# Kernel tuning notes

Measured on AMD Instinct MI355X. Metric: run time of the kernel, lower is better.

## Reference

```python
import jax, jax.numpy as jnp
import numpy as np

B, T, D, H, OUT = 1024, 2048, 5, 64, 128


def _lstm_layer(x, Wih, Whh, bih, bhh):
    """PyTorch-convention LSTM layer. x: [B,T,Din]; gate order i,f,g,o."""
    b, t = x.shape[0], x.shape[1]
    h = Whh.shape[1]
    # Precompute input projections for all timesteps (the only big GEMM).
    xp = jnp.einsum('btd,gd->btg', x, Wih) + bih + bhh        # [B,T,4H]
    xp = jnp.swapaxes(xp, 0, 1)                               # [T,B,4H]

    def step(carry, xt):
        hprev, cprev = carry
        gates = xt + hprev @ Whh.T                            # [B,4H]
        i, f, g, o = jnp.split(gates, 4, axis=-1)
        i = jax.nn.sigmoid(i)
        f = jax.nn.sigmoid(f)
        g = jnp.tanh(g)
        o = jax.nn.sigmoid(o)
        c = f * cprev + i * g
        hnew = o * jnp.tanh(c)
        return (hnew, c), hnew

    h0 = jnp.zeros((b, h), x.dtype)
    (hT, cT), hs = jax.lax.scan(step, (h0, h0), xp)
    return jnp.swapaxes(hs, 0, 1), hT                         # [B,T,H], [B,H]


def setup_inputs() -> dict:
    key = jax.random.key(0)
    ks = jax.random.split(key, 11)
    s = 1.0 / np.sqrt(H)  # PyTorch LSTM init range

    def u(k, shape):
        return jax.random.uniform(k, shape, jnp.float32, -s, s)

    return {
        'x': jax.random.normal(ks[0], (B, T, D), jnp.float32),
        'W_ih0': u(ks[1], (4 * H, D)),
        'W_hh0': u(ks[2], (4 * H, H)),
        'b_ih0': u(ks[3], (4 * H,)),
        'b_hh0': u(ks[4], (4 * H,)),
        'W_ih1': u(ks[5], (4 * H, H)),
        'W_hh1': u(ks[6], (4 * H, H)),
        'b_ih1': u(ks[7], (4 * H,)),
        'b_hh1': u(ks[8], (4 * H,)),
        'W_fc': u(ks[9], (OUT, H)),
        'b_fc': u(ks[10], (OUT,)),
    }


def reference(x, W_ih0, W_hh0, b_ih0, b_hh0, W_ih1, W_hh1, b_ih1, b_hh1, W_fc, b_fc):
    # Layer 1 over raw 5-dim signal; inter-layer dropout is inactive at inference.
    y1, _ = _lstm_layer(x, W_ih0, W_hh0, b_ih0, b_hh0)
    # Layer 2; only its final hidden state hn[-1] is used downstream.
    _, h2 = _lstm_layer(y1, W_ih1, W_hh1, b_ih1, b_hh1)
    return jax.nn.relu(h2 @ W_fc.T + b_fc)                    # [B,128]
```

## Files before the change

kernel.cpp:

```cpp
#include <hip/hip_runtime.h>
#include <math.h>

#define BATCH 1024
#define TSEQ  2048
#define DIN   5
#define H     64
#define BT    4
#define SSTR  144
#define NOUT  128

typedef _Float16 f16x8 __attribute__((ext_vector_type(8)));
typedef float    f32x4 __attribute__((ext_vector_type(4)));

#if __has_builtin(__builtin_amdgcn_rcpf)
__device__ __forceinline__ float rcp_fast(float x) { return __builtin_amdgcn_rcpf(x); }
#else
__device__ __forceinline__ float rcp_fast(float x) { return 1.0f / x; }
#endif

#define LOG2E 1.44269504088896f

__device__ __forceinline__ float sigm2(float s) {
    return rcp_fast(1.0f + __builtin_amdgcn_exp2f(-s));
}
__device__ __forceinline__ float tanh2(float s) {
    return fmaf(-2.0f, rcp_fast(__builtin_amdgcn_exp2f(s) + 1.0f), 1.0f);
}

__global__ __launch_bounds__(512)
void lstm_mfma(const float* __restrict__ x,
               const float* __restrict__ Wih0, const float* __restrict__ Whh0,
               const float* __restrict__ bih0, const float* __restrict__ bhh0,
               const float* __restrict__ Wih1, const float* __restrict__ Whh1,
               const float* __restrict__ bih1, const float* __restrict__ bhh1,
               const float* __restrict__ Wfc,  const float* __restrict__ bfc,
               float* __restrict__ out)
{
    __shared__ alignas(16) _Float16 S[2][BT * SSTR];
    __shared__ alignas(16) float    h2f[BT][H];

    const int tid  = threadIdx.x;
    const int w    = tid >> 6;
    const int lane = tid & 63;
    const int col  = lane & 15;
    const int q    = lane >> 4;
    const int ww   = w & 3;
    const int lay  = w >> 2;
    const int hu   = 16 * ww + col;
    const int b0   = blockIdx.x * BT;

    for (int j = tid; j < 2 * BT * SSTR; j += 512)
        ((_Float16*)S)[j] = (_Float16)0.0f;

    const float sgl[4] = {LOG2E, LOG2E, 2.0f * LOG2E, LOG2E};

    f16x8 Bf[4][4];
    f32x4 bC[4];
    #pragma unroll
    for (int g = 0; g < 4; ++g) {
        const int   row = g * 64 + hu;
        const float sg  = sgl[g];
        const float* Wa = lay ? (Wih1 + row * H) : (Whh0 + row * H);
        f16x8 f0, f1, f2, f3;
        #pragma unroll
        for (int j = 0; j < 8; ++j) {
            f0[j] = (_Float16)(Wa[q * 8 + j] * sg);
            f1[j] = (_Float16)(Wa[32 + q * 8 + j] * sg);
        }
        if (lay) {
            const float* Wb = Whh1 + row * H;
            #pragma unroll
            for (int j = 0; j < 8; ++j) {
                f2[j] = (_Float16)(Wb[q * 8 + j] * sg);
                f3[j] = (_Float16)(Wb[32 + q * 8 + j] * sg);
            }
        } else {
            #pragma unroll
            for (int j = 0; j < 8; ++j) {
                const int kk = q * 8 + j;
                f2[j] = (_Float16)(kk < DIN ? Wih0[row * DIN + kk] * sg : 0.0f);
                f3[j] = (_Float16)0.0f;
            }
        }
        Bf[g][0] = f0; Bf[g][1] = f1; Bf[g][2] = f2; Bf[g][3] = f3;
        const float bb = (lay ? (bih1[row] + bhh1[row])
                              : (bih0[row] + bhh0[row])) * sg;
        bC[g] = f32x4{bb, bb, bb, bb};
    }

    const float* xp = x + (size_t)(b0 + (col >> 2)) * TSEQ * DIN;
    f16x8 ax = {(_Float16)0.0f, (_Float16)0.0f, (_Float16)0.0f, (_Float16)0.0f,
                (_Float16)0.0f, (_Float16)0.0f, (_Float16)0.0f, (_Float16)0.0f};
    f32x4 dx[4];
    if (lay == 0) {
        if (q == 0) {
            ax[0] = (_Float16)xp[0]; ax[1] = (_Float16)xp[1];
            ax[2] = (_Float16)xp[2]; ax[3] = (_Float16)xp[3];
            ax[4] = (_Float16)xp[4];
        }
        #pragma unroll
        for (int g = 0; g < 4; ++g)
            dx[g] = __builtin_amdgcn_mfma_f32_16x16x32_f16(ax, Bf[g][2], bC[g], 0, 0, 0);
        xp += DIN;
    }

    const int ab  = (col >> 2) * SSTR + q * 8;
    const int wb1 = q * SSTR + hu;
    const int wb2 = q * SSTR + 64 + hu;
    float cst = 0.0f, h2fin = 0.0f;

    __syncthreads();

    #pragma unroll 1
    for (int i = 0; i <= TSEQ; ++i) {
        const _Float16* rb = S[(i + 1) & 1];
        _Float16*       wbuf = S[i & 1];

        if (lay == 0) {
            const bool xld = (q == 0) && (i + 1 < TSEQ);
            float x0, x1, x2, x3, x4;
            if (xld) { x0 = xp[0]; x1 = xp[1]; x2 = xp[2]; x3 = xp[3]; x4 = xp[4]; }

            f16x8 a0 = *(const f16x8*)&rb[ab];
            f16x8 a1 = *(const f16x8*)&rb[ab + 32];
            f32x4 d[4];
            #pragma unroll
            for (int g = 0; g < 4; ++g) {
                d[g] = __builtin_amdgcn_mfma_f32_16x16x32_f16(a0, Bf[g][0], dx[g], 0, 0, 0);
                d[g] = __builtin_amdgcn_mfma_f32_16x16x32_f16(a1, Bf[g][1], d[g], 0, 0, 0);
            }
            if (i < TSEQ) {
                float iv = sigm2(d[0][0]);
                float fv = sigm2(d[1][0]);
                float gv = tanh2(d[2][0]);
                float ov = sigm2(d[3][0]);
                cst = fmaf(fv, cst, iv * gv);
                wbuf[wb1] = (_Float16)(ov * tanh2(2.0f * LOG2E * cst));
            }
            if (xld) {
                ax[0] = (_Float16)x0; ax[1] = (_Float16)x1;
                ax[2] = (_Float16)x2; ax[3] = (_Float16)x3;
                ax[4] = (_Float16)x4;
            }
            #pragma unroll
            for (int g = 0; g < 4; ++g)
                dx[g] = __builtin_amdgcn_mfma_f32_16x16x32_f16(ax, Bf[g][2], bC[g], 0, 0, 0);
            xp += DIN;
        } else {
            f16x8 ay0 = *(const f16x8*)&rb[ab];
            f16x8 ay1 = *(const f16x8*)&rb[ab + 32];
            f16x8 ah0 = *(const f16x8*)&rb[ab + 64];
            f16x8 ah1 = *(const f16x8*)&rb[ab + 96];
            f32x4 d[4];
            #pragma unroll
            for (int g = 0; g < 4; ++g) {
                d[g] = __builtin_amdgcn_mfma_f32_16x16x32_f16(ay0, Bf[g][0], bC[g], 0, 0, 0);
                d[g] = __builtin_amdgcn_mfma_f32_16x16x32_f16(ay1, Bf[g][1], d[g], 0, 0, 0);
                d[g] = __builtin_amdgcn_mfma_f32_16x16x32_f16(ah0, Bf[g][2], d[g], 0, 0, 0);
                d[g] = __builtin_amdgcn_mfma_f32_16x16x32_f16(ah1, Bf[g][3], d[g], 0, 0, 0);
            }
            if (i > 0) {
                float iv = sigm2(d[0][0]);
                float fv = sigm2(d[1][0]);
                float gv = tanh2(d[2][0]);
                float ov = sigm2(d[3][0]);
                cst = fmaf(fv, cst, iv * gv);
                h2fin = ov * tanh2(2.0f * LOG2E * cst);
                wbuf[wb2] = (_Float16)h2fin;
            }
        }
        __syncthreads();
    }

    if (lay) h2f[q][hu] = h2fin;
    __syncthreads();
    {
        const int e = tid >> 7;
        const int o = tid & (NOUT - 1);
        const float4* wr = (const float4*)(Wfc + o * H);
        const float*  hv = h2f[e];
        float s0 = 0.f, s1 = 0.f, s2 = 0.f, s3 = 0.f;
        #pragma unroll
        for (int k = 0; k < H / 4; ++k) {
            float4 wv = wr[k];
            s0 = fmaf(wv.x, hv[4 * k + 0], s0);
            s1 = fmaf(wv.y, hv[4 * k + 1], s1);
            s2 = fmaf(wv.z, hv[4 * k + 2], s2);
            s3 = fmaf(wv.w, hv[4 * k + 3], s3);
        }
        float acc = bfc[o] + (s0 + s1) + (s2 + s3);
        out[(size_t)(b0 + e) * NOUT + o] = fmaxf(acc, 0.0f);
    }
}

extern "C" void kernel_launch(void* const* d_in, const int* in_sizes, int n_in,
                              void* d_out, int out_size, void* d_ws, size_t ws_size,
                              hipStream_t stream) {
    const float* x    = (const float*)d_in[0];
    const float* Wih0 = (const float*)d_in[1];
    const float* Whh0 = (const float*)d_in[2];
    const float* bih0 = (const float*)d_in[3];
    const float* bhh0 = (const float*)d_in[4];
    const float* Wih1 = (const float*)d_in[5];
    const float* Whh1 = (const float*)d_in[6];
    const float* bih1 = (const float*)d_in[7];
    const float* bhh1 = (const float*)d_in[8];
    const float* Wfc  = (const float*)d_in[9];
    const float* bfc  = (const float*)d_in[10];
    float* out = (float*)d_out;

    lstm_mfma<<<dim3(BATCH / BT), dim3(512), 0, stream>>>(
        x, Wih0, Whh0, bih0, bhh0, Wih1, Whh1, bih1, bhh1, Wfc, bfc, out);
}
```

Before: 979.1 us.

## Merge both LSTM layers into each wave, halving block size to 256 threads

Instead of dedicating four waves to layer 1 and four to layer 2, each of four waves now computes both layers' gates for its hidden units in the same wavefront-pipelined step. Each wave holds all weight fragments in registers and issues the layer-1, layer-2 input and layer-2 recurrent MFMAs as independent chains, and the x loads are reorganized. This halves the waves per block, aiming to cut barrier cost and let the MFMA chains overlap within a wave. In exchange it raises register pressure and per-wave serial work, and the launch bound of one block per SIMD may limit occupancy.

```diff
diff --git a/kernel.cpp b/kernel.cpp
--- a/kernel.cpp
+++ b/kernel.cpp
@@ -19,6 +19,7 @@
 #endif
 
 #define LOG2E 1.44269504088896f
+#define MFMA16(A, B, C) __builtin_amdgcn_mfma_f32_16x16x32_f16((A), (B), (C), 0, 0, 0)
 
 __device__ __forceinline__ float sigm2(float s) {
     return rcp_fast(1.0f + __builtin_amdgcn_exp2f(-s));
@@ -27,7 +28,7 @@
     return fmaf(-2.0f, rcp_fast(__builtin_amdgcn_exp2f(s) + 1.0f), 1.0f);
 }
 
-__global__ __launch_bounds__(512)
+__global__ __launch_bounds__(256, 1)
 void lstm_mfma(const float* __restrict__ x,
                const float* __restrict__ Wih0, const float* __restrict__ Whh0,
                const float* __restrict__ bih0, const float* __restrict__ bhh0,
@@ -40,156 +41,140 @@
     __shared__ alignas(16) float    h2f[BT][H];
 
     const int tid  = threadIdx.x;
-    const int w    = tid >> 6;
+    const int ww   = tid >> 6;
     const int lane = tid & 63;
     const int col  = lane & 15;
     const int q    = lane >> 4;
-    const int ww   = w & 3;
-    const int lay  = w >> 2;
     const int hu   = 16 * ww + col;
     const int b0   = blockIdx.x * BT;
 
-    for (int j = tid; j < 2 * BT * SSTR; j += 512)
+    for (int j = tid; j < 2 * BT * SSTR; j += 256)
         ((_Float16*)S)[j] = (_Float16)0.0f;
 
     const float sgl[4] = {LOG2E, LOG2E, 2.0f * LOG2E, LOG2E};
 
-    f16x8 Bf[4][4];
-    f32x4 bC[4];
+    f16x8 Bh[4][2];
+    f16x8 Bx[4];
+    f16x8 C2[4][4];
+    f32x4 bC1[4], bC2[4];
     #pragma unroll
     for (int g = 0; g < 4; ++g) {
         const int   row = g * 64 + hu;
         const float sg  = sgl[g];
-        const float* Wa = lay ? (Wih1 + row * H) : (Whh0 + row * H);
-        f16x8 f0, f1, f2, f3;
+        const float* wh0 = Whh0 + row * H;
+        const float* wi1 = Wih1 + row * H;
+        const float* wh1 = Whh1 + row * H;
         #pragma unroll
         for (int j = 0; j < 8; ++j) {
-            f0[j] = (_Float16)(Wa[q * 8 + j] * sg);
-            f1[j] = (_Float16)(Wa[32 + q * 8 + j] * sg);
+            const int k = q * 8 + j;
+            Bh[g][0][j] = (_Float16)(wh0[k]      * sg);
+            Bh[g][1][j] = (_Float16)(wh0[32 + k] * sg);
+            C2[g][0][j] = (_Float16)(wi1[k]      * sg);
+            C2[g][1][j] = (_Float16)(wi1[32 + k] * sg);
+            C2[g][2][j] = (_Float16)(wh1[k]      * sg);
+            C2[g][3][j] = (_Float16)(wh1[32 + k] * sg);
+            Bx[g][j]    = (_Float16)(k < DIN ? Wih0[row * DIN + k] * sg : 0.0f);
         }
-        if (lay) {
-            const float* Wb = Whh1 + row * H;
-            #pragma unroll
-            for (int j = 0; j < 8; ++j) {
-                f2[j] = (_Float16)(Wb[q * 8 + j] * sg);
-                f3[j] = (_Float16)(Wb[32 + q * 8 + j] * sg);
-            }
-        } else {
-            #pragma unroll
-            for (int j = 0; j < 8; ++j) {
-                const int kk = q * 8 + j;
-                f2[j] = (_Float16)(kk < DIN ? Wih0[row * DIN + kk] * sg : 0.0f);
-                f3[j] = (_Float16)0.0f;
-            }
-        }
-        Bf[g][0] = f0; Bf[g][1] = f1; Bf[g][2] = f2; Bf[g][3] = f3;
-        const float bb = (lay ? (bih1[row] + bhh1[row])
-                              : (bih0[row] + bhh0[row])) * sg;
-        bC[g] = f32x4{bb, bb, bb, bb};
+        const float b1 = (bih0[row] + bhh0[row]) * sg;
+        const float b2 = (bih1[row] + bhh1[row]) * sg;
+        bC1[g] = f32x4{b1, b1, b1, b1};
+        bC2[g] = f32x4{b2, b2, b2, b2};
     }
 
     const float* xp = x + (size_t)(b0 + (col >> 2)) * TSEQ * DIN;
+    float x0 = 0.f, x1 = 0.f, x2 = 0.f, x3 = 0.f, x4 = 0.f;
+    if (q == 0) { x0 = xp[0]; x1 = xp[1]; x2 = xp[2]; x3 = xp[3]; x4 = xp[4]; }
+    xp += DIN;
+
     f16x8 ax = {(_Float16)0.0f, (_Float16)0.0f, (_Float16)0.0f, (_Float16)0.0f,
                 (_Float16)0.0f, (_Float16)0.0f, (_Float16)0.0f, (_Float16)0.0f};
-    f32x4 dx[4];
-    if (lay == 0) {
-        if (q == 0) {
-            ax[0] = (_Float16)xp[0]; ax[1] = (_Float16)xp[1];
-            ax[2] = (_Float16)xp[2]; ax[3] = (_Float16)xp[3];
-            ax[4] = (_Float16)xp[4];
-        }
-        #pragma unroll
-        for (int g = 0; g < 4; ++g)
-            dx[g] = __builtin_amdgcn_mfma_f32_16x16x32_f16(ax, Bf[g][2], bC[g], 0, 0, 0);
-        xp += DIN;
-    }
 
     const int ab  = (col >> 2) * SSTR + q * 8;
     const int wb1 = q * SSTR + hu;
     const int wb2 = q * SSTR + 64 + hu;
-    float cst = 0.0f, h2fin = 0.0f;
+    float cst1 = 0.f, cst2 = 0.f, h2fin = 0.f;
 
     __syncthreads();
 
     #pragma unroll 1
     for (int i = 0; i <= TSEQ; ++i) {
-        const _Float16* rb = S[(i + 1) & 1];
+        const _Float16* rb   = S[(i + 1) & 1];
         _Float16*       wbuf = S[i & 1];
 
-        if (lay == 0) {
-            const bool xld = (q == 0) && (i + 1 < TSEQ);
-            float x0, x1, x2, x3, x4;
-            if (xld) { x0 = xp[0]; x1 = xp[1]; x2 = xp[2]; x3 = xp[3]; x4 = xp[4]; }
+        f16x8 a0  = *(const f16x8*)&rb[ab];
+        f16x8 a1  = *(const f16x8*)&rb[ab + 32];
+        f16x8 ah0 = *(const f16x8*)&rb[ab + 64];
+        f16x8 ah1 = *(const f16x8*)&rb[ab + 96];
 
-            f16x8 a0 = *(const f16x8*)&rb[ab];
-            f16x8 a1 = *(const f16x8*)&rb[ab + 32];
-            f32x4 d[4];
-            #pragma unroll
-            for (int g = 0; g < 4; ++g) {
-                d[g] = __builtin_amdgcn_mfma_f32_16x16x32_f16(a0, Bf[g][0], dx[g], 0, 0, 0);
-                d[g] = __builtin_amdgcn_mfma_f32_16x16x32_f16(a1, Bf[g][1], d[g], 0, 0, 0);
-            }
-            if (i < TSEQ) {
-                float iv = sigm2(d[0][0]);
-                float fv = sigm2(d[1][0]);
-                float gv = tanh2(d[2][0]);
-                float ov = sigm2(d[3][0]);
-                cst = fmaf(fv, cst, iv * gv);
-                wbuf[wb1] = (_Float16)(ov * tanh2(2.0f * LOG2E * cst));
-            }
-            if (xld) {
-                ax[0] = (_Float16)x0; ax[1] = (_Float16)x1;
-                ax[2] = (_Float16)x2; ax[3] = (_Float16)x3;
-                ax[4] = (_Float16)x4;
-            }
-            #pragma unroll
-            for (int g = 0; g < 4; ++g)
-                dx[g] = __builtin_amdgcn_mfma_f32_16x16x32_f16(ax, Bf[g][2], bC[g], 0, 0, 0);
-            xp += DIN;
-        } else {
-            f16x8 ay0 = *(const f16x8*)&rb[ab];
-            f16x8 ay1 = *(const f16x8*)&rb[ab + 32];
-            f16x8 ah0 = *(const f16x8*)&rb[ab + 64];
-            f16x8 ah1 = *(const f16x8*)&rb[ab + 96];
-            f32x4 d[4];
-            #pragma unroll
-            for (int g = 0; g < 4; ++g) {
-                d[g] = __builtin_amdgcn_mfma_f32_16x16x32_f16(ay0, Bf[g][0], bC[g], 0, 0, 0);
-                d[g] = __builtin_amdgcn_mfma_f32_16x16x32_f16(ay1, Bf[g][1], d[g], 0, 0, 0);
-                d[g] = __builtin_amdgcn_mfma_f32_16x16x32_f16(ah0, Bf[g][2], d[g], 0, 0, 0);
-                d[g] = __builtin_amdgcn_mfma_f32_16x16x32_f16(ah1, Bf[g][3], d[g], 0, 0, 0);
-            }
-            if (i > 0) {
-                float iv = sigm2(d[0][0]);
-                float fv = sigm2(d[1][0]);
-                float gv = tanh2(d[2][0]);
-                float ov = sigm2(d[3][0]);
-                cst = fmaf(fv, cst, iv * gv);
-                h2fin = ov * tanh2(2.0f * LOG2E * cst);
-                wbuf[wb2] = (_Float16)h2fin;
-            }
+        if (q == 0) {
+            ax[0] = (_Float16)x0; ax[1] = (_Float16)x1; ax[2] = (_Float16)x2;
+            ax[3] = (_Float16)x3; ax[4] = (_Float16)x4;
+        }
+        f32x4 dx[4];
+        #pragma unroll
+        for (int g = 0; g < 4; ++g)
+            dx[g] = MFMA16(ax, Bx[g], bC1[g]);
+
+        if (q == 0 && i + 1 < TSEQ) { x0 = xp[0]; x1 = xp[1]; x2 = xp[2]; x3 = xp[3]; x4 = xp[4]; }
+        xp += DIN;
+
+        f32x4 d[4], e2[4], f2[4];
+        const f32x4 z4 = {0.f, 0.f, 0.f, 0.f};
+        #pragma unroll
+        for (int g = 0; g < 4; ++g) {
+            d[g]  = MFMA16(a0,  Bh[g][0], dx[g]);
+            d[g]  = MFMA16(a1,  Bh[g][1], d[g]);
+            e2[g] = MFMA16(a0,  C2[g][0], bC2[g]);
+            e2[g] = MFMA16(a1,  C2[g][1], e2[g]);
+            f2[g] = MFMA16(ah0, C2[g][2], z4);
+            f2[g] = MFMA16(ah1, C2[g][3], f2[g]);
+        }
+
+        if (i < TSEQ) {
+            float iv = sigm2(d[0][0]);
+            float fv = sigm2(d[1][0]);
+            float gv = tanh2(d[2][0]);
+            float ov = sigm2(d[3][0]);
+            cst1 = fmaf(fv, cst1, iv * gv);
+            wbuf[wb1] = (_Float16)(ov * tanh2(2.0f * LOG2E * cst1));
+        }
+        if (i > 0) {
+            float p0 = e2[0][0] + f2[0][0];
+            float p1 = e2[1][0] + f2[1][0];
+            float p2 = e2[2][0] + f2[2][0];
+            float p3 = e2[3][0] + f2[3][0];
+            float iv = sigm2(p0);
+            float fv = sigm2(p1);
+            float gv = tanh2(p2);
+            float ov = sigm2(p3);
+            cst2 = fmaf(fv, cst2, iv * gv);
+            h2fin = ov * tanh2(2.0f * LOG2E * cst2);
+            wbuf[wb2] = (_Float16)h2fin;
         }
         __syncthreads();
     }
 
-    if (lay) h2f[q][hu] = h2fin;
+    h2f[q][hu] = h2fin;
     __syncthreads();
     {
-        const int e = tid >> 7;
-        const int o = tid & (NOUT - 1);
+        const int o  = tid & (NOUT - 1);
+        const int eh = tid >> 7;
         const float4* wr = (const float4*)(Wfc + o * H);
-        const float*  hv = h2f[e];
-        float s0 = 0.f, s1 = 0.f, s2 = 0.f, s3 = 0.f;
         #pragma unroll
-        for (int k = 0; k < H / 4; ++k) {
-            float4 wv = wr[k];
-            s0 = fmaf(wv.x, hv[4 * k + 0], s0);
-            s1 = fmaf(wv.y, hv[4 * k + 1], s1);
-            s2 = fmaf(wv.z, hv[4 * k + 2], s2);
-            s3 = fmaf(wv.w, hv[4 * k + 3], s3);
+        for (int e = eh; e < BT; e += 2) {
+            const float* hv = h2f[e];
+            float s0 = 0.f, s1 = 0.f, s2 = 0.f, s3 = 0.f;
+            #pragma unroll
+            for (int k = 0; k < H / 4; ++k) {
+                float4 wv = wr[k];
+                s0 = fmaf(wv.x, hv[4 * k + 0], s0);
+                s1 = fmaf(wv.y, hv[4 * k + 1], s1);
+                s2 = fmaf(wv.z, hv[4 * k + 2], s2);
+                s3 = fmaf(wv.w, hv[4 * k + 3], s3);
+            }
+            float acc = bfc[o] + (s0 + s1) + (s2 + s3);
+            out[(size_t)(b0 + e) * NOUT + o] = fmaxf(acc, 0.0f);
         }
-        float acc = bfc[o] + (s0 + s1) + (s2 + s3);
-        out[(size_t)(b0 + e) * NOUT + o] = fmaxf(acc, 0.0f);
     }
 }
 
@@ -209,6 +194,6 @@
     const float* bfc  = (const float*)d_in[10];
     float* out = (float*)d_out;
 
-    lstm_mfma<<<dim3(BATCH / BT), dim3(512), 0, stream>>>(
+    lstm_mfma<<<dim3(BATCH / BT), dim3(256), 0, stream>>>(
         x, Wih0, Whh0, bih0, bhh0, Wih1, Whh1, bih1, bhh1, Wfc, bfc, out);
 }
```

Result: slower. 1.452 ms (+48.3%).

## Compute layer-1 input projection with scalar FMAs and lighten per-step barrier

Applied to the files above, without the earlier changes.

Layer 0 no longer spends four extra MFMAs per step on the 5-wide input projection. Each lane now loads the x values for its own batch row and computes the gate pre-activation with five scalar FMAs, then injects the result into the MFMA accumulator. MFMA sections are wrapped in s_setprio raises, and __syncthreads is replaced by an explicit lgkmcnt wait plus s_barrier so outstanding global memory ops are not waited on. This trims the serial per-timestep critical path, at the cost of every lane issuing x loads and holding the 20 wx weights in registers.

```diff
diff --git a/kernel.cpp b/kernel.cpp
--- a/kernel.cpp
+++ b/kernel.cpp
@@ -19,12 +19,19 @@
 #endif
 
 #define LOG2E 1.44269504088896f
+#define MFMA16(A, B, C) __builtin_amdgcn_mfma_f32_16x16x32_f16((A), (B), (C), 0, 0, 0)
 
 __device__ __forceinline__ float sigm2(float s) {
     return rcp_fast(1.0f + __builtin_amdgcn_exp2f(-s));
 }
 __device__ __forceinline__ float tanh2(float s) {
     return fmaf(-2.0f, rcp_fast(__builtin_amdgcn_exp2f(s) + 1.0f), 1.0f);
+}
+
+__device__ __forceinline__ void sync_lgkm() {
+    asm volatile("s_waitcnt lgkmcnt(0)" ::: "memory");
+    __builtin_amdgcn_s_barrier();
+    asm volatile("" ::: "memory");
 }
 
 __global__ __launch_bounds__(512)
@@ -56,52 +63,45 @@
 
     f16x8 Bf[4][4];
     f32x4 bC[4];
+    float wx[4][DIN];
+    float b1s[4];
     #pragma unroll
     for (int g = 0; g < 4; ++g) {
         const int   row = g * 64 + hu;
         const float sg  = sgl[g];
-        const float* Wa = lay ? (Wih1 + row * H) : (Whh0 + row * H);
-        f16x8 f0, f1, f2, f3;
-        #pragma unroll
-        for (int j = 0; j < 8; ++j) {
-            f0[j] = (_Float16)(Wa[q * 8 + j] * sg);
-            f1[j] = (_Float16)(Wa[32 + q * 8 + j] * sg);
+        if (lay) {
+            const float* wa = Wih1 + row * H;
+            const float* wb = Whh1 + row * H;
+            #pragma unroll
+            for (int j = 0; j < 8; ++j) {
+                const int k = q * 8 + j;
+                Bf[g][0][j] = (_Float16)(wa[k]      * sg);
+                Bf[g][1][j] = (_Float16)(wa[32 + k] * sg);
+                Bf[g][2][j] = (_Float16)(wb[k]      * sg);
+                Bf[g][3][j] = (_Float16)(wb[32 + k] * sg);
+            }
+            const float bb = (bih1[row] + bhh1[row]) * sg;
+            bC[g] = f32x4{bb, bb, bb, bb};
+        } else {
+            const float* wh = Whh0 + row * H;
+            #pragma unroll
+            for (int j = 0; j < 8; ++j) {
+                const int k = q * 8 + j;
+                Bf[g][0][j] = (_Float16)(wh[k]      * sg);
+                Bf[g][1][j] = (_Float16)(wh[32 + k] * sg);
+            }
+            #pragma unroll
+            for (int j = 0; j < DIN; ++j)
+                wx[g][j] = Wih0[row * DIN + j] * sg;
+            b1s[g] = (bih0[row] + bhh0[row]) * sg;
         }
-        if (lay) {
-            const float* Wb = Whh1 + row * H;
-            #pragma unroll
-            for (int j = 0; j < 8; ++j) {
-                f2[j] = (_Float16)(Wb[q * 8 + j] * sg);
-                f3[j] = (_Float16)(Wb[32 + q * 8 + j] * sg);
-            }
-        } else {
-            #pragma unroll
-            for (int j = 0; j < 8; ++j) {
-                const int kk = q * 8 + j;
-                f2[j] = (_Float16)(kk < DIN ? Wih0[row * DIN + kk] * sg : 0.0f);
-                f3[j] = (_Float16)0.0f;
-            }
-        }
-        Bf[g][0] = f0; Bf[g][1] = f1; Bf[g][2] = f2; Bf[g][3] = f3;
-        const float bb = (lay ? (bih1[row] + bhh1[row])
-                              : (bih0[row] + bhh0[row])) * sg;
-        bC[g] = f32x4{bb, bb, bb, bb};
-    }
-
-    const float* xp = x + (size_t)(b0 + (col >> 2)) * TSEQ * DIN;
-    f16x8 ax = {(_Float16)0.0f, (_Float16)0.0f, (_Float16)0.0f, (_Float16)0.0f,
-                (_Float16)0.0f, (_Float16)0.0f, (_Float16)0.0f, (_Float16)0.0f};
-    f32x4 dx[4];
+    }
+
+    const float* xq = x + (size_t)(b0 + q) * TSEQ * DIN;
+    float x0 = 0.f, x1 = 0.f, x2 = 0.f, x3 = 0.f, x4 = 0.f;
     if (lay == 0) {
-        if (q == 0) {
-            ax[0] = (_Float16)xp[0]; ax[1] = (_Float16)xp[1];
-            ax[2] = (_Float16)xp[2]; ax[3] = (_Float16)xp[3];
-            ax[4] = (_Float16)xp[4];
-        }
-        #pragma unroll
-        for (int g = 0; g < 4; ++g)
-            dx[g] = __builtin_amdgcn_mfma_f32_16x16x32_f16(ax, Bf[g][2], bC[g], 0, 0, 0);
-        xp += DIN;
+        x0 = xq[0]; x1 = xq[1]; x2 = xq[2]; x3 = xq[3]; x4 = xq[4];
+        xq += DIN;
     }
 
     const int ab  = (col >> 2) * SSTR + q * 8;
@@ -113,22 +113,37 @@
 
     #pragma unroll 1
     for (int i = 0; i <= TSEQ; ++i) {
-        const _Float16* rb = S[(i + 1) & 1];
+        const _Float16* rb   = S[(i + 1) & 1];
         _Float16*       wbuf = S[i & 1];
 
         if (lay == 0) {
-            const bool xld = (q == 0) && (i + 1 < TSEQ);
-            float x0, x1, x2, x3, x4;
-            if (xld) { x0 = xp[0]; x1 = xp[1]; x2 = xp[2]; x3 = xp[3]; x4 = xp[4]; }
+            const bool ld = (i + 1 < TSEQ);
+            float n0, n1, n2, n3, n4;
+            if (ld) { n0 = xq[0]; n1 = xq[1]; n2 = xq[2]; n3 = xq[3]; n4 = xq[4]; xq += DIN; }
 
             f16x8 a0 = *(const f16x8*)&rb[ab];
             f16x8 a1 = *(const f16x8*)&rb[ab + 32];
+
+            float dxs[4];
+            #pragma unroll
+            for (int g = 0; g < 4; ++g) {
+                float s = fmaf(x0, wx[g][0], b1s[g]);
+                s = fmaf(x1, wx[g][1], s);
+                s = fmaf(x2, wx[g][2], s);
+                s = fmaf(x3, wx[g][3], s);
+                dxs[g] = fmaf(x4, wx[g][4], s);
+            }
+
             f32x4 d[4];
+            __builtin_amdgcn_s_setprio(1);
             #pragma unroll
             for (int g = 0; g < 4; ++g) {
-                d[g] = __builtin_amdgcn_mfma_f32_16x16x32_f16(a0, Bf[g][0], dx[g], 0, 0, 0);
-                d[g] = __builtin_amdgcn_mfma_f32_16x16x32_f16(a1, Bf[g][1], d[g], 0, 0, 0);
-            }
+                f32x4 c0 = {dxs[g], 0.f, 0.f, 0.f};
+                d[g] = MFMA16(a0, Bf[g][0], c0);
+                d[g] = MFMA16(a1, Bf[g][1], d[g]);
+            }
+            __builtin_amdgcn_s_setprio(0);
+
             if (i < TSEQ) {
                 float iv = sigm2(d[0][0]);
                 float fv = sigm2(d[1][0]);
@@ -137,28 +152,22 @@
                 cst = fmaf(fv, cst, iv * gv);
                 wbuf[wb1] = (_Float16)(ov * tanh2(2.0f * LOG2E * cst));
             }
-            if (xld) {
-                ax[0] = (_Float16)x0; ax[1] = (_Float16)x1;
-                ax[2] = (_Float16)x2; ax[3] = (_Float16)x3;
-                ax[4] = (_Float16)x4;
-            }
-            #pragma unroll
-            for (int g = 0; g < 4; ++g)
-                dx[g] = __builtin_amdgcn_mfma_f32_16x16x32_f16(ax, Bf[g][2], bC[g], 0, 0, 0);
-            xp += DIN;
+            if (ld) { x0 = n0; x1 = n1; x2 = n2; x3 = n3; x4 = n4; }
         } else {
             f16x8 ay0 = *(const f16x8*)&rb[ab];
             f16x8 ay1 = *(const f16x8*)&rb[ab + 32];
             f16x8 ah0 = *(const f16x8*)&rb[ab + 64];
             f16x8 ah1 = *(const f16x8*)&rb[ab + 96];
             f32x4 d[4];
+            __builtin_amdgcn_s_setprio(1);
             #pragma unroll
             for (int g = 0; g < 4; ++g) {
-                d[g] = __builtin_amdgcn_mfma_f32_16x16x32_f16(ay0, Bf[g][0], bC[g], 0, 0, 0);
-                d[g] = __builtin_amdgcn_mfma_f32_16x16x32_f16(ay1, Bf[g][1], d[g], 0, 0, 0);
-                d[g] = __builtin_amdgcn_mfma_f32_16x16x32_f16(ah0, Bf[g][2], d[g], 0, 0, 0);
-                d[g] = __builtin_amdgcn_mfma_f32_16x16x32_f16(ah1, Bf[g][3], d[g], 0, 0, 0);
-            }
+                d[g] = MFMA16(ay0, Bf[g][0], bC[g]);
+                d[g] = MFMA16(ay1, Bf[g][1], d[g]);
+                d[g] = MFMA16(ah0, Bf[g][2], d[g]);
+                d[g] = MFMA16(ah1, Bf[g][3], d[g]);
+            }
+            __builtin_amdgcn_s_setprio(0);
             if (i > 0) {
                 float iv = sigm2(d[0][0]);
                 float fv = sigm2(d[1][0]);
@@ -169,7 +178,7 @@
                 wbuf[wb2] = (_Float16)h2fin;
             }
         }
-        __syncthreads();
+        sync_lgkm();
     }
 
     if (lay) h2f[q][hu] = h2fin;
```

New measurement: 1.003 ms. 1.02x slower.
